# Kernel optimization log

Hardware: AMD Instinct MI355X
Metric: run time of the kernel (lower is better)

The kernel has to match this reference:

```python
import jax, jax.numpy as jnp
import numpy as np

B, T, V, E, H, K = 128, 512, 50257, 100, 128, 12
START, STOP = 10, 11


def setup_inputs() -> dict:
    key = jax.random.key(0)
    ks = jax.random.split(key, 11)
    sentences = jax.random.randint(ks[0], (B, T), 0, V)
    h0 = jax.random.normal(ks[1], (B, H), jnp.float32)
    c0 = jax.random.normal(ks[2], (B, H), jnp.float32)
    embed = jax.random.normal(ks[3], (V, E), jnp.float32) * 0.1
    Wih = jax.random.normal(ks[4], (4 * H, E), jnp.float32) * 0.1   # torch gate order i,f,g,o
    Whh = jax.random.normal(ks[5], (4 * H, H), jnp.float32) * 0.1
    bih = jax.random.normal(ks[6], (4 * H,), jnp.float32) * 0.1
    bhh = jax.random.normal(ks[7], (4 * H,), jnp.float32) * 0.1
    Wtag = jax.random.normal(ks[8], (K, H), jnp.float32) * 0.1
    btag = jax.random.normal(ks[9], (K,), jnp.float32) * 0.1
    transitions = jax.random.normal(ks[10], (K, K), jnp.float32)
    transitions = transitions.at[START, :].set(-10000.0).at[:, STOP].set(-10000.0)
    return dict(sentences=sentences, h0=h0, c0=c0, embed=embed,
                Wih=Wih, Whh=Whh, bih=bih, bhh=bhh,
                Wtag=Wtag, btag=btag, transitions=transitions)


def reference(sentences, h0, c0, embed, Wih, Whh, bih, bhh, Wtag, btag, transitions):
    # --- embedding + single-layer LSTM (batch_first); dropout is identity at eval ---
    x = embed[sentences]                       # [B, T, E]
    x_t = jnp.swapaxes(x, 0, 1)                # [T, B, E]

    def lstm_step(carry, xt):
        h, c = carry
        gates = xt @ Wih.T + h @ Whh.T + bih + bhh      # [B, 4H]
        i, f, g, o = jnp.split(gates, 4, axis=-1)
        c = jax.nn.sigmoid(f) * c + jax.nn.sigmoid(i) * jnp.tanh(g)
        h = jax.nn.sigmoid(o) * jnp.tanh(c)
        return (h, c), h

    _, hs = jax.lax.scan(lstm_step, (h0, c0), x_t)      # hs: [T, B, H]
    emissions = hs @ Wtag.T + btag                      # [T, B, K]

    # --- batched Viterbi DP over time ---
    def vit_step(prev, emit):
        # prev: [B, K] trellis at t-1; transitions[i, j] = score(i -> j)
        v = prev[:, :, None] + transitions[None]        # [B, K, K]
        best = jnp.max(v, axis=1)                       # [B, K]
        bp = jnp.argmax(v, axis=1).astype(jnp.int32)    # [B, K]
        return emit + best, bp

    last, bps = jax.lax.scan(vit_step, emissions[0], emissions[1:])  # bps: [T-1, B, K]
    scores = jnp.max(last, axis=-1)                     # [B]
    last_tag = jnp.argmax(last, axis=-1).astype(jnp.int32)  # [B]

    # --- backtrace (reverse scan) ---
    def back_step(tag, bp):
        prev = jnp.take_along_axis(bp, tag[:, None], axis=1)[:, 0]
        return prev, prev

    _, early_tags = jax.lax.scan(back_step, last_tag, bps, reverse=True)  # [T-1, B]
    paths = jnp.concatenate([early_tags, last_tag[None]], axis=0)         # [T, B]
    paths = jnp.swapaxes(paths, 0, 1)                                     # [B, T]
    return scores, paths
```

## Files before the change

kernel.cpp:

```cpp
#include <hip/hip_runtime.h>
#include <hip/hip_bf16.h>

#define BB 128
#define TT 512
#define EE 100
#define HH 128
#define KK 12
#define VV 50257
#define NB 8
#define NBLK 16

typedef short bf16x8 __attribute__((ext_vector_type(8)));
typedef float f32x4  __attribute__((ext_vector_type(4)));

__device__ __forceinline__ unsigned short f2bf(float x) {
  __hip_bfloat16 h = __float2bfloat16(x);
  return *reinterpret_cast<unsigned short*>(&h);
}
__device__ __forceinline__ float bf2f(unsigned short u) {
  return __uint_as_float(((unsigned)u) << 16);
}

__device__ __forceinline__ bf16x8 load8_bf(const float* p) {
  float4 a = *reinterpret_cast<const float4*>(p);
  float4 b = *reinterpret_cast<const float4*>(p + 4);
  bf16x8 r;
  r[0] = (short)f2bf(a.x); r[1] = (short)f2bf(a.y);
  r[2] = (short)f2bf(a.z); r[3] = (short)f2bf(a.w);
  r[4] = (short)f2bf(b.x); r[5] = (short)f2bf(b.y);
  r[6] = (short)f2bf(b.z); r[7] = (short)f2bf(b.w);
  return r;
}

__device__ __forceinline__ bf16x8 load8_bf_pad_bias(const float* row, int k0,
                                                    float bias) {
  bf16x8 r;
  #pragma unroll
  for (int i = 0; i < 8; ++i) {
    int k = k0 + i;
    unsigned short v = 0;
    if (k < EE) v = f2bf(row[k]);
    else if (k == EE) v = f2bf(bias);
    r[i] = (short)v;
  }
  return r;
}

__device__ __forceinline__ int frag_idx(int b, int k) {
  return ((k >> 5) << 9) + ((b + (((k >> 3) & 3) << 4)) << 3) + (k & 7);
}

__global__ __launch_bounds__(256) void precast_kernel(
    const float* __restrict__ embed, unsigned short* __restrict__ ebf)
{
  int id = blockIdx.x * 256 + threadIdx.x;
  if (id >= VV * 16) return;
  int v = id >> 4, g = id & 15;
  const float* row = embed + (size_t)v * EE;
  bf16x8 o;
  #pragma unroll
  for (int i = 0; i < 8; ++i) {
    int k = g * 8 + i;
    unsigned short u = 0;
    if (k < EE) u = f2bf(row[k]);
    else if (k == EE) u = 0x3F80;
    o[i] = (short)u;
  }
  *reinterpret_cast<bf16x8*>(ebf + (size_t)id * 8) = o;
}

__global__ __launch_bounds__(256) void wprep_kernel(
    const float* __restrict__ Wih, const float* __restrict__ bih,
    const float* __restrict__ bhh, unsigned short* __restrict__ wbf)
{
  int id = blockIdx.x * 256 + threadIdx.x;
  if (id >= 8 * 4 * 4 * 64) return;
  int l = id & 63, kt = (id >> 6) & 3, tt = (id >> 8) & 3, s8 = id >> 10;
  int gcol = tt * HH + 16 * s8 + (l & 15);
  int k0 = kt * 32 + (l >> 4) * 8;
  float bias = bih[gcol] + bhh[gcol];
  bf16x8 r = load8_bf_pad_bias(Wih + (size_t)gcol * EE, k0, bias);
  *reinterpret_cast<bf16x8*>(wbf + (size_t)id * 8) = r;
}

__global__ __launch_bounds__(256, 2) void pregates_kernel(
    const int* __restrict__ sent, const unsigned short* __restrict__ ebf,
    const unsigned short* __restrict__ wbf, unsigned short* __restrict__ P16)
{
  const int w = threadIdx.x >> 6, l = threadIdx.x & 63;
  const int c = l & 15, q = l >> 4;
  const int rt = blockIdx.x * 4 + w;
  const int flat = rt * 16 + c;
  const int b = flat >> 9, t = flat & 511;
  const int id = sent[b * TT + t];

  bf16x8 xa[4];
  #pragma unroll
  for (int kt = 0; kt < 4; ++kt)
    xa[kt] = *reinterpret_cast<const bf16x8*>(
        ebf + (size_t)id * 128 + kt * 32 + q * 8);

  const bf16x8* wb = reinterpret_cast<const bf16x8*>(wbf);
  #pragma unroll
  for (int s8 = 0; s8 < 8; ++s8) {
    f32x4 acc[4];
    #pragma unroll
    for (int tt = 0; tt < 4; ++tt) {
      f32x4 z = {0.f, 0.f, 0.f, 0.f};
      acc[tt] = z;
    }
    #pragma unroll
    for (int kt = 0; kt < 4; ++kt) {
      #pragma unroll
      for (int tt = 0; tt < 4; ++tt)
        acc[tt] = __builtin_amdgcn_mfma_f32_16x16x32_bf16(
            xa[kt], wb[((s8 * 4 + tt) * 4 + kt) * 64 + l], acc[tt], 0, 0, 0);
    }
    const int e = s8 * 16 + c;
    #pragma unroll
    for (int r4 = 0; r4 < 4; ++r4) {
      int fr = rt * 16 + q * 4 + r4;
      ushort4 o = make_ushort4(f2bf(acc[0][r4]), f2bf(acc[1][r4]),
                               f2bf(acc[2][r4]), f2bf(acc[3][r4]));
      *reinterpret_cast<ushort4*>(P16 + ((size_t)fr * 128 + e) * 4) = o;
    }
  }
}

__global__ __launch_bounds__(512, 2) void lstm_kernel(
    const unsigned short* __restrict__ P16, const float* __restrict__ Whh,
    const float* __restrict__ h0, const float* __restrict__ c0,
    unsigned short* __restrict__ hst)
{
  __shared__ __align__(16) unsigned short hfrag[2][2048];
  __shared__ __align__(16) unsigned int lpad[7168];

  const int bg  = blockIdx.x;
  const int tid = threadIdx.x;
  const int w   = tid >> 6;
  const int l   = tid & 63;
  const int c   = l & 15;
  const int q   = l >> 4;
  const int ew  = 16 * w + c;

  bf16x8 wh[4][4];
  #pragma unroll
  for (int tt = 0; tt < 4; ++tt) {
    const int gcol = tt * HH + ew;
    #pragma unroll
    for (int kt = 0; kt < 4; ++kt)
      wh[tt][kt] = load8_bf(Whh + (size_t)gcol * HH + kt * 32 + q * 8);
  }

  float cst[2];
  #pragma unroll
  for (int r = 0; r < 2; ++r)
    cst[r] = c0[(size_t)(bg * NB + q * 2 + r) * HH + ew];

  {
    int4 z = {0, 0, 0, 0};
    reinterpret_cast<int4*>(hfrag)[tid] = z;
  }
  for (int i = tid; i < 7168; i += 512) lpad[i] = 0u;
  unsigned int keep = lpad[tid];
  asm volatile("" :: "v"(keep));
  __syncthreads();

  for (int idx = tid; idx < NB * HH; idx += 512) {
    int lb = idx >> 7, k = idx & 127;
    int row = ((lb >> 1) << 2) + (lb & 1);
    hfrag[0][frag_idx(row, k)] = f2bf(h0[(size_t)(bg * NB + lb) * HH + k]);
  }

  const unsigned short* pb0 =
      P16 + (size_t)(bg * NB + q * 2 + 0) * (TT * 512) + ew * 4;
  const unsigned short* pb1 =
      P16 + (size_t)(bg * NB + q * 2 + 1) * (TT * 512) + ew * 4;
  ushort4 pA[2], pB[2];
  pA[0] = *reinterpret_cast<const ushort4*>(pb0);
  pA[1] = *reinterpret_cast<const ushort4*>(pb1);
  pB[0] = *reinterpret_cast<const ushort4*>(pb0 + 512);
  pB[1] = *reinterpret_cast<const ushort4*>(pb1 + 512);

  unsigned short hp[2] = {0, 0};
  unsigned short* hb0 = hst + (size_t)(bg * NB + q * 2 + 0) * TT * HH + ew;
  unsigned short* hb1 = hst + (size_t)(bg * NB + q * 2 + 1) * TT * HH + ew;

  const int hw_off = frag_idx(q * 4, ew);
  __syncthreads();

  auto step = [&](int s, ushort4 (&pcur)[2]) {
    const int rb = s & 1;

    if (s >= 1 && s <= TT) {
      hb0[(size_t)(s - 1) * HH] = hp[0];
      hb1[(size_t)(s - 1) * HH] = hp[1];
    }

    if (s < TT) {
      bf16x8 ha[4];
      const bf16x8* hr = reinterpret_cast<const bf16x8*>(&hfrag[rb][0]) + l;
      #pragma unroll
      for (int kt = 0; kt < 4; ++kt) ha[kt] = hr[kt * 64];

      f32x4 acc[4];
      #pragma unroll
      for (int tt = 0; tt < 4; ++tt) {
        f32x4 z = {0.f, 0.f, 0.f, 0.f};
        acc[tt] = z;
      }
      acc[0][0] = bf2f(pcur[0].x); acc[1][0] = bf2f(pcur[0].y);
      acc[2][0] = bf2f(pcur[0].z); acc[3][0] = bf2f(pcur[0].w);
      acc[0][1] = bf2f(pcur[1].x); acc[1][1] = bf2f(pcur[1].y);
      acc[2][1] = bf2f(pcur[1].z); acc[3][1] = bf2f(pcur[1].w);

      if (s + 2 < TT) {
        pcur[0] = *reinterpret_cast<const ushort4*>(pb0 + (size_t)(s + 2) * 512);
        pcur[1] = *reinterpret_cast<const ushort4*>(pb1 + (size_t)(s + 2) * 512);
      }

      #pragma unroll
      for (int kt = 0; kt < 4; ++kt) {
        #pragma unroll
        for (int tt = 0; tt < 4; ++tt)
          acc[tt] = __builtin_amdgcn_mfma_f32_16x16x32_bf16(ha[kt], wh[tt][kt], acc[tt], 0, 0, 0);
      }

      unsigned short* hwp = &hfrag[rb ^ 1][hw_off];
      #pragma unroll
      for (int r = 0; r < 2; ++r) {
        float ai  = __builtin_amdgcn_exp2f(acc[0][r] * -1.44269504f);
        float bgg = __builtin_amdgcn_exp2f(acc[2][r] * -2.88539008f);
        float af  = __builtin_amdgcn_exp2f(acc[1][r] * -1.44269504f);
        float ao  = __builtin_amdgcn_exp2f(acc[3][r] * -1.44269504f);
        float sitg = (1.0f - bgg) *
                     __builtin_amdgcn_rcpf((1.0f + ai) * (1.0f + bgg));
        float sf = __builtin_amdgcn_rcpf(1.0f + af);
        cst[r] = __fmaf_rn(sf, cst[r], sitg);
        float cc = fminf(fmaxf(cst[r], -30.0f), 30.0f);
        float ec = __builtin_amdgcn_exp2f(cc * -2.88539008f);
        float hv = (1.0f - ec) *
                   __builtin_amdgcn_rcpf((1.0f + ao) * (1.0f + ec));
        unsigned short hu = f2bf(hv);
        hwp[r * 8] = hu;
        hp[r] = hu;
      }
    }
    __syncthreads();
  };

  for (int s = 0; s < TT + 2; s += 2) {
    step(s, pA);
    step(s + 1, pB);
  }
}

__global__ __launch_bounds__(256, 2) void emis_kernel(
    const unsigned short* __restrict__ hst, const float* __restrict__ Wtag,
    const float* __restrict__ btag, float* __restrict__ E)
{
  const int w = threadIdx.x >> 6, l = threadIdx.x & 63;
  const int c = l & 15, q = l >> 4;
  const int rt = blockIdx.x * 4 + w;

  bf16x8 we[4];
  #pragma unroll
  for (int kt = 0; kt < 4; ++kt) {
    #pragma unroll
    for (int i = 0; i < 8; ++i) we[kt][i] = 0;
  }
  float bt = 0.f;
  if (c < KK) {
    #pragma unroll
    for (int kt = 0; kt < 4; ++kt)
      we[kt] = load8_bf(Wtag + (size_t)c * HH + kt * 32 + q * 8);
    bt = btag[c];
  }

  bf16x8 ha[4];
  #pragma unroll
  for (int kt = 0; kt < 4; ++kt)
    ha[kt] = *reinterpret_cast<const bf16x8*>(
        hst + (size_t)(rt * 16 + c) * HH + kt * 32 + q * 8);

  f32x4 acc = {0.f, 0.f, 0.f, 0.f};
  #pragma unroll
  for (int kt = 0; kt < 4; ++kt)
    acc = __builtin_amdgcn_mfma_f32_16x16x32_bf16(ha[kt], we[kt], acc, 0, 0, 0);

  #pragma unroll
  for (int r = 0; r < 4; ++r)
    E[(size_t)(rt * 16 + q * 4 + r) * 16 + c] = acc[r] + bt;
}

__global__ __launch_bounds__(64) void vit_kernel(
    const float* __restrict__ E, const float* __restrict__ trans,
    float* __restrict__ out)
{
  __shared__ __align__(16) float trl[KK * 16];
  __shared__ __align__(16) float vit[16];
  __shared__ unsigned char bp[TT * KK];
  __shared__ unsigned char path[TT];

  const int b = blockIdx.x, tid = threadIdx.x;
  if (tid < KK * KK) {
    int i = tid / KK, jj = tid - i * KK;
    trl[jj * 16 + i] = trans[tid];
  }
  __syncthreads();

  const int j = tid;
  const float* Eb = E + (size_t)b * TT * 16 + j;

  float cur[8], nxt[8];
  if (j < 16) {
    #pragma unroll
    for (int i = 0; i < 8; ++i) cur[i] = Eb[i * 16];
  }

  for (int tb = 0; tb < TT; tb += 8) {
    if (j < 16 && tb + 8 < TT) {
      #pragma unroll
      for (int i = 0; i < 8; ++i) nxt[i] = Eb[(size_t)(tb + 8 + i) * 16];
    }
    #pragma unroll
    for (int i = 0; i < 8; ++i) {
      const int t = tb + i;
      if (j < KK) {
        float Ev = cur[i];
        float nv;
        if (t == 0) {
          nv = Ev;
        } else {
          float4 v0 = *reinterpret_cast<const float4*>(&vit[0]);
          float4 v1 = *reinterpret_cast<const float4*>(&vit[4]);
          float4 v2 = *reinterpret_cast<const float4*>(&vit[8]);
          float4 t0 = *reinterpret_cast<const float4*>(&trl[j * 16]);
          float4 t1 = *reinterpret_cast<const float4*>(&trl[j * 16 + 4]);
          float4 t2 = *reinterpret_cast<const float4*>(&trl[j * 16 + 8]);
          float cand[KK] = {v0.x + t0.x, v0.y + t0.y, v0.z + t0.z, v0.w + t0.w,
                            v1.x + t1.x, v1.y + t1.y, v1.z + t1.z, v1.w + t1.w,
                            v2.x + t2.x, v2.y + t2.y, v2.z + t2.z, v2.w + t2.w};
          float g0 = fmaxf(fmaxf(cand[0], cand[1]), cand[2]);
          float g1 = fmaxf(fmaxf(cand[3], cand[4]), cand[5]);
          float g2 = fmaxf(fmaxf(cand[6], cand[7]), cand[8]);
          float g3 = fmaxf(fmaxf(cand[9], cand[10]), cand[11]);
          float best = fmaxf(fmaxf(g0, g1), fmaxf(g2, g3));
          int bi = 11;
          #pragma unroll
          for (int k = 10; k >= 0; --k) bi = (cand[k] == best) ? k : bi;
          nv = Ev + best;
          bp[t * KK + j] = (unsigned char)bi;
        }
        vit[j] = nv;
      }
      __syncthreads();
    }
    #pragma unroll
    for (int i = 0; i < 8; ++i) cur[i] = nxt[i];
  }

  if (tid == 0) {
    float best = vit[0];
    int tag = 0;
    for (int jj = 1; jj < KK; ++jj)
      if (vit[jj] > best) { best = vit[jj]; tag = jj; }
    out[b] = best;
    path[TT - 1] = (unsigned char)tag;
    for (int t = TT - 1; t >= 1; --t) {
      tag = bp[t * KK + tag];
      path[t - 1] = (unsigned char)tag;
    }
  }
  __syncthreads();

  #pragma unroll
  for (int i = 0; i < 8; ++i)
    out[BB + (size_t)b * TT + tid + i * 64] = (float)path[tid + i * 64];
}

extern "C" void kernel_launch(void* const* d_in, const int* in_sizes, int n_in,
                              void* d_out, int out_size, void* d_ws, size_t ws_size,
                              hipStream_t stream) {
  const int*   sent  = (const int*)d_in[0];
  const float* h0    = (const float*)d_in[1];
  const float* c0    = (const float*)d_in[2];
  const float* embed = (const float*)d_in[3];
  const float* Wih   = (const float*)d_in[4];
  const float* Whh   = (const float*)d_in[5];
  const float* bih   = (const float*)d_in[6];
  const float* bhh   = (const float*)d_in[7];
  const float* Wtag  = (const float*)d_in[8];
  const float* btag  = (const float*)d_in[9];
  const float* trans = (const float*)d_in[10];
  float* out = (float*)d_out;

  unsigned short* ebf = (unsigned short*)d_ws;
  unsigned short* wbf = ebf + (size_t)VV * 128;
  unsigned short* P16 = wbf + 8192 * 8;
  unsigned short* hst = P16 + (size_t)BB * TT * 512;
  float*          Ebf = (float*)(hst + (size_t)BB * TT * HH);

  precast_kernel<<<(VV * 16 + 255) / 256, 256, 0, stream>>>(embed, ebf);
  wprep_kernel<<<32, 256, 0, stream>>>(Wih, bih, bhh, wbf);
  pregates_kernel<<<(BB * TT / 16) / 4, 256, 0, stream>>>(sent, ebf, wbf, P16);
  lstm_kernel<<<NBLK, 512, 0, stream>>>(P16, Whh, h0, c0, hst);
  emis_kernel<<<(BB * TT / 16) / 4, 256, 0, stream>>>(hst, Wtag, btag, Ebf);
  vit_kernel<<<BB, 64, 0, stream>>>(Ebf, trans, out);
}
```

Before: 533.9 us.

## Fuse prep kernels and emissions into Viterbi, lighten LSTM barrier

Merges the embedding precast and weight prep into one launch, and folds the emission MFMA into the Viterbi kernel so emissions are computed per 16-step chunk into shared memory instead of a global round trip. In the LSTM kernel, __syncthreads is replaced by a raw lgkmcnt wait plus s_barrier, the clamp becomes a single fmed3, and the LDS padding array is enlarged, which further lowers occupancy. The intent is to remove two launches, the emission buffer traffic and per-step barrier overhead. The trade-offs are extra syncs in the Viterbi loop and a barrier that does not wait on vector memory.

```diff
diff --git a/kernel.cpp b/kernel.cpp
--- a/kernel.cpp
+++ b/kernel.cpp
@@ -9,6 +9,7 @@
 #define VV 50257
 #define NB 8
 #define NBLK 16
+#define NPRE ((VV * 16 + 255) / 256)
 
 typedef short bf16x8 __attribute__((ext_vector_type(8)));
 typedef float f32x4  __attribute__((ext_vector_type(4)));
@@ -50,37 +51,40 @@
   return ((k >> 5) << 9) + ((b + (((k >> 3) & 3) << 4)) << 3) + (k & 7);
 }
 
-__global__ __launch_bounds__(256) void precast_kernel(
-    const float* __restrict__ embed, unsigned short* __restrict__ ebf)
+__device__ __forceinline__ void lds_barrier() {
+  asm volatile("s_waitcnt lgkmcnt(0)\n\ts_barrier" ::: "memory");
+}
+
+__global__ __launch_bounds__(256) void prep_kernel(
+    const float* __restrict__ embed, const float* __restrict__ Wih,
+    const float* __restrict__ bih, const float* __restrict__ bhh,
+    unsigned short* __restrict__ ebf, unsigned short* __restrict__ wbf)
 {
-  int id = blockIdx.x * 256 + threadIdx.x;
-  if (id >= VV * 16) return;
-  int v = id >> 4, g = id & 15;
-  const float* row = embed + (size_t)v * EE;
-  bf16x8 o;
-  #pragma unroll
-  for (int i = 0; i < 8; ++i) {
-    int k = g * 8 + i;
-    unsigned short u = 0;
-    if (k < EE) u = f2bf(row[k]);
-    else if (k == EE) u = 0x3F80;
-    o[i] = (short)u;
-  }
-  *reinterpret_cast<bf16x8*>(ebf + (size_t)id * 8) = o;
-}
-
-__global__ __launch_bounds__(256) void wprep_kernel(
-    const float* __restrict__ Wih, const float* __restrict__ bih,
-    const float* __restrict__ bhh, unsigned short* __restrict__ wbf)
-{
-  int id = blockIdx.x * 256 + threadIdx.x;
-  if (id >= 8 * 4 * 4 * 64) return;
-  int l = id & 63, kt = (id >> 6) & 3, tt = (id >> 8) & 3, s8 = id >> 10;
-  int gcol = tt * HH + 16 * s8 + (l & 15);
-  int k0 = kt * 32 + (l >> 4) * 8;
-  float bias = bih[gcol] + bhh[gcol];
-  bf16x8 r = load8_bf_pad_bias(Wih + (size_t)gcol * EE, k0, bias);
-  *reinterpret_cast<bf16x8*>(wbf + (size_t)id * 8) = r;
+  if (blockIdx.x < NPRE) {
+    int id = blockIdx.x * 256 + threadIdx.x;
+    if (id >= VV * 16) return;
+    int v = id >> 4, g = id & 15;
+    const float* row = embed + (size_t)v * EE;
+    bf16x8 o;
+    #pragma unroll
+    for (int i = 0; i < 8; ++i) {
+      int k = g * 8 + i;
+      unsigned short u = 0;
+      if (k < EE) u = f2bf(row[k]);
+      else if (k == EE) u = 0x3F80;
+      o[i] = (short)u;
+    }
+    *reinterpret_cast<bf16x8*>(ebf + (size_t)id * 8) = o;
+  } else {
+    int id = (blockIdx.x - NPRE) * 256 + threadIdx.x;
+    if (id >= 8 * 4 * 4 * 64) return;
+    int l = id & 63, kt = (id >> 6) & 3, tt = (id >> 8) & 3, s8 = id >> 10;
+    int gcol = tt * HH + 16 * s8 + (l & 15);
+    int k0 = kt * 32 + (l >> 4) * 8;
+    float bias = bih[gcol] + bhh[gcol];
+    bf16x8 r = load8_bf_pad_bias(Wih + (size_t)gcol * EE, k0, bias);
+    *reinterpret_cast<bf16x8*>(wbf + (size_t)id * 8) = r;
+  }
 }
 
 __global__ __launch_bounds__(256, 2) void pregates_kernel(
@@ -133,7 +137,7 @@
     unsigned short* __restrict__ hst)
 {
   __shared__ __align__(16) unsigned short hfrag[2][2048];
-  __shared__ __align__(16) unsigned int lpad[7168];
+  __shared__ __align__(16) unsigned int lpad[19456];
 
   const int bg  = blockIdx.x;
   const int tid = threadIdx.x;
@@ -161,7 +165,7 @@
     int4 z = {0, 0, 0, 0};
     reinterpret_cast<int4*>(hfrag)[tid] = z;
   }
-  for (int i = tid; i < 7168; i += 512) lpad[i] = 0u;
+  for (int i = tid; i < 19456; i += 512) lpad[i] = 0u;
   unsigned int keep = lpad[tid];
   asm volatile("" :: "v"(keep));
   __syncthreads();
@@ -237,7 +241,7 @@
                      __builtin_amdgcn_rcpf((1.0f + ai) * (1.0f + bgg));
         float sf = __builtin_amdgcn_rcpf(1.0f + af);
         cst[r] = __fmaf_rn(sf, cst[r], sitg);
-        float cc = fminf(fmaxf(cst[r], -30.0f), 30.0f);
+        float cc = __builtin_amdgcn_fmed3f(cst[r], -30.0f, 30.0f);
         float ec = __builtin_amdgcn_exp2f(cc * -2.88539008f);
         float hv = (1.0f - ec) *
                    __builtin_amdgcn_rcpf((1.0f + ao) * (1.0f + ec));
@@ -246,7 +250,7 @@
         hp[r] = hu;
       }
     }
-    __syncthreads();
+    lds_barrier();
   };
 
   for (int s = 0; s < TT + 2; s += 2) {
@@ -255,13 +259,24 @@
   }
 }
 
-__global__ __launch_bounds__(256, 2) void emis_kernel(
+__global__ __launch_bounds__(64) void vit_kernel(
     const unsigned short* __restrict__ hst, const float* __restrict__ Wtag,
-    const float* __restrict__ btag, float* __restrict__ E)
+    const float* __restrict__ btag, const float* __restrict__ trans,
+    float* __restrict__ out)
 {
-  const int w = threadIdx.x >> 6, l = threadIdx.x & 63;
-  const int c = l & 15, q = l >> 4;
-  const int rt = blockIdx.x * 4 + w;
+  __shared__ __align__(16) float trl[KK * 16];
+  __shared__ __align__(16) float vbuf[16];
+  __shared__ __align__(16) float ering[16 * 16];
+  __shared__ unsigned char bp[TT * KK];
+  __shared__ unsigned char path[TT];
+
+  const int b = blockIdx.x, tid = threadIdx.x;
+  const int c = tid & 15, q = tid >> 4;
+
+  if (tid < KK * KK) {
+    int i = tid / KK, jj = tid - i * KK;
+    trl[jj * 16 + i] = trans[tid];
+  }
 
   bf16x8 we[4];
   #pragma unroll
@@ -276,65 +291,38 @@
       we[kt] = load8_bf(Wtag + (size_t)c * HH + kt * 32 + q * 8);
     bt = btag[c];
   }
-
-  bf16x8 ha[4];
-  #pragma unroll
-  for (int kt = 0; kt < 4; ++kt)
-    ha[kt] = *reinterpret_cast<const bf16x8*>(
-        hst + (size_t)(rt * 16 + c) * HH + kt * 32 + q * 8);
-
-  f32x4 acc = {0.f, 0.f, 0.f, 0.f};
-  #pragma unroll
-  for (int kt = 0; kt < 4; ++kt)
-    acc = __builtin_amdgcn_mfma_f32_16x16x32_bf16(ha[kt], we[kt], acc, 0, 0, 0);
-
-  #pragma unroll
-  for (int r = 0; r < 4; ++r)
-    E[(size_t)(rt * 16 + q * 4 + r) * 16 + c] = acc[r] + bt;
-}
-
-__global__ __launch_bounds__(64) void vit_kernel(
-    const float* __restrict__ E, const float* __restrict__ trans,
-    float* __restrict__ out)
-{
-  __shared__ __align__(16) float trl[KK * 16];
-  __shared__ __align__(16) float vit[16];
-  __shared__ unsigned char bp[TT * KK];
-  __shared__ unsigned char path[TT];
-
-  const int b = blockIdx.x, tid = threadIdx.x;
-  if (tid < KK * KK) {
-    int i = tid / KK, jj = tid - i * KK;
-    trl[jj * 16 + i] = trans[tid];
-  }
+  const unsigned short* hb = hst + (size_t)b * TT * HH;
   __syncthreads();
 
-  const int j = tid;
-  const float* Eb = E + (size_t)b * TT * 16 + j;
-
-  float cur[8], nxt[8];
-  if (j < 16) {
-    #pragma unroll
-    for (int i = 0; i < 8; ++i) cur[i] = Eb[i * 16];
-  }
-
-  for (int tb = 0; tb < TT; tb += 8) {
-    if (j < 16 && tb + 8 < TT) {
-      #pragma unroll
-      for (int i = 0; i < 8; ++i) nxt[i] = Eb[(size_t)(tb + 8 + i) * 16];
-    }
-    #pragma unroll
-    for (int i = 0; i < 8; ++i) {
+  for (int tb = 0; tb < TT; tb += 16) {
+    bf16x8 ha[4];
+    #pragma unroll
+    for (int kt = 0; kt < 4; ++kt)
+      ha[kt] = *reinterpret_cast<const bf16x8*>(
+          hb + (size_t)(tb + c) * HH + kt * 32 + q * 8);
+    f32x4 accE = {0.f, 0.f, 0.f, 0.f};
+    #pragma unroll
+    for (int kt = 0; kt < 4; ++kt)
+      accE = __builtin_amdgcn_mfma_f32_16x16x32_bf16(ha[kt], we[kt], accE, 0, 0, 0);
+    __syncthreads();
+    #pragma unroll
+    for (int r = 0; r < 4; ++r)
+      ering[(q * 4 + r) * 16 + c] = accE[r] + bt;
+    __syncthreads();
+
+    #pragma unroll
+    for (int i = 0; i < 16; ++i) {
       const int t = tb + i;
-      if (j < KK) {
-        float Ev = cur[i];
+      if (tid < KK) {
+        const int j = tid;
+        float Ev = ering[i * 16 + j];
         float nv;
         if (t == 0) {
           nv = Ev;
         } else {
-          float4 v0 = *reinterpret_cast<const float4*>(&vit[0]);
-          float4 v1 = *reinterpret_cast<const float4*>(&vit[4]);
-          float4 v2 = *reinterpret_cast<const float4*>(&vit[8]);
+          float4 v0 = *reinterpret_cast<const float4*>(&vbuf[0]);
+          float4 v1 = *reinterpret_cast<const float4*>(&vbuf[4]);
+          float4 v2 = *reinterpret_cast<const float4*>(&vbuf[8]);
           float4 t0 = *reinterpret_cast<const float4*>(&trl[j * 16]);
           float4 t1 = *reinterpret_cast<const float4*>(&trl[j * 16 + 4]);
           float4 t2 = *reinterpret_cast<const float4*>(&trl[j * 16 + 8]);
@@ -352,19 +340,17 @@
           nv = Ev + best;
           bp[t * KK + j] = (unsigned char)bi;
         }
-        vit[j] = nv;
+        vbuf[j] = nv;
       }
       __syncthreads();
     }
-    #pragma unroll
-    for (int i = 0; i < 8; ++i) cur[i] = nxt[i];
   }
 
   if (tid == 0) {
-    float best = vit[0];
+    float best = vbuf[0];
     int tag = 0;
     for (int jj = 1; jj < KK; ++jj)
-      if (vit[jj] > best) { best = vit[jj]; tag = jj; }
+      if (vbuf[jj] > best) { best = vbuf[jj]; tag = jj; }
     out[b] = best;
     path[TT - 1] = (unsigned char)tag;
     for (int t = TT - 1; t >= 1; --t) {
@@ -399,12 +385,9 @@
   unsigned short* wbf = ebf + (size_t)VV * 128;
   unsigned short* P16 = wbf + 8192 * 8;
   unsigned short* hst = P16 + (size_t)BB * TT * 512;
-  float*          Ebf = (float*)(hst + (size_t)BB * TT * HH);
-
-  precast_kernel<<<(VV * 16 + 255) / 256, 256, 0, stream>>>(embed, ebf);
-  wprep_kernel<<<32, 256, 0, stream>>>(Wih, bih, bhh, wbf);
+
+  prep_kernel<<<NPRE + 32, 256, 0, stream>>>(embed, Wih, bih, bhh, ebf, wbf);
   pregates_kernel<<<(BB * TT / 16) / 4, 256, 0, stream>>>(sent, ebf, wbf, P16);
   lstm_kernel<<<NBLK, 512, 0, stream>>>(P16, Whh, h0, c0, hst);
-  emis_kernel<<<(BB * TT / 16) / 4, 256, 0, stream>>>(hst, Wtag, btag, Ebf);
-  vit_kernel<<<BB, 64, 0, stream>>>(Ebf, trans, out);
-}
+  vit_kernel<<<BB, 64, 0, stream>>>(hst, Wtag, btag, trans, out);
+}
```

Result: no change. 530.8 us (-0.6%).
